# Performance work log

Hardware: AMD Instinct MI355X
Metric: run time of the kernel (lower is better)

The kernel has to match this reference:

```python
import jax, jax.numpy as jnp
import numpy as np

NUM_HEADS = 16
LN_EPS = 1e-5


def _layer_norm(x, g, b):
    m = x.mean(-1, keepdims=True)
    v = x.var(-1, keepdims=True)
    return (x - m) / jnp.sqrt(v + LN_EPS) * g + b


def setup_inputs() -> dict:
    key = jax.random.key(0)
    ks = jax.random.split(key, 4)
    Bq, Bk, Nk, C = 128, 128, 256, 1024
    return {
        "qx": jax.random.normal(ks[0], (Bq, 1, C), jnp.float32),
        "kx": jax.random.normal(ks[1], (Bk, Nk, C), jnp.float32),
        "gq": jnp.ones((C,), jnp.float32),
        "bq": jnp.zeros((C,), jnp.float32),
        "gk": jnp.ones((C,), jnp.float32),
        "bk": jnp.zeros((C,), jnp.float32),
        "Wq": jax.random.normal(ks[2], (C, C), jnp.float32) * (C ** -0.5),
        "Wk": jax.random.normal(ks[3], (C, C), jnp.float32) * (C ** -0.5),
    }


def reference(qx, kx, gq, bq, gk, bk, Wq, Wk):
    H = NUM_HEADS
    Bq, _, C = qx.shape  # qx: [Bq, 1, C]
    Bk, Nk, _ = kx.shape  # kx: [Bk, Nk, C]
    hd = C // H
    scale = hd ** -0.5
    # LayerNorm + linear projections (nn.Linear: x @ W.T, no bias)
    q = (_layer_norm(qx, gq, bq) @ Wq.T).reshape(Bq, H, hd)       # [Bq, H, hd] (Nq=1 squeezed)
    k = (_layer_norm(kx, gk, bk) @ Wk.T).reshape(Bk, Nk, H, hd)   # [Bk, Nk, H, hd]
    # Full bipartite cross-batch attention scores: [Bq, Bk, H, Nk]
    attn = jnp.einsum('qhc,knhc->qkhn', q, k) * scale
    attn = jax.nn.softmax(attn, axis=-1)
    # v = kx broadcast over heads in original einsum 'khnc,qkhn->qkc';
    # equivalent: sum attn over heads, then contract over Nk.
    w = attn.sum(axis=2)                                           # [Bq, Bk, Nk]
    x = jnp.einsum('knc,qkn->qkc', kx, w)                          # [Bq, Bk, C]
    return x
```

## Files before the change

kernel.cpp:

```cpp
#include <hip/hip_runtime.h>


typedef unsigned short ushort_t;
typedef __bf16 bf16x8 __attribute__((ext_vector_type(8)));
typedef float f32x4 __attribute__((ext_vector_type(4)));

#define AS1 __attribute__((address_space(1)))
#define AS3 __attribute__((address_space(3)))

__device__ __forceinline__ void gload_lds16(const void* g, void* l) {
  __builtin_amdgcn_global_load_lds((const AS1 unsigned int*)g, (AS3 unsigned int*)l, 16, 0, 0);
}

__device__ __forceinline__ ushort_t f2bf(float f) {
  unsigned u = __float_as_uint(f);
  unsigned r = u + 0x7FFFu + ((u >> 16) & 1u);
  return (ushort_t)(r >> 16);
}

__global__ __launch_bounds__(256) void cvt_bf16_kernel(const float* __restrict__ src,
                                                       ushort_t* __restrict__ dst, int n4) {
  int i = blockIdx.x * 256 + threadIdx.x;
  if (i < n4) {
    float4 v = ((const float4*)src)[i];
    ushort4 o;
    o.x = f2bf(v.x); o.y = f2bf(v.y); o.z = f2bf(v.z); o.w = f2bf(v.w);
    ((ushort4*)dst)[i] = o;
  }
}

__global__ __launch_bounds__(256) void ln_kernel(const float* __restrict__ kx,
                                                 const float* __restrict__ qx,
                                                 const float* __restrict__ gk,
                                                 const float* __restrict__ bk,
                                                 const float* __restrict__ gq,
                                                 const float* __restrict__ bq,
                                                 const float* __restrict__ WqF,
                                                 ushort_t* __restrict__ kln,
                                                 ushort_t* __restrict__ qproj) {
  const int tid = threadIdx.x, lane = tid & 63, wid = tid >> 6;

  if (blockIdx.x < 128) {
    const int ti = blockIdx.x * 4 + wid;
    const int mq = ti >> 6, nq = ti & 63;
    const int g = lane >> 4, rr = lane & 15;

    float s = 0.f, s2 = 0.f;
    {
      const float* p = qx + (size_t)(mq * 16 + (lane & 15)) * 1024 + (lane >> 4) * 256;
      #pragma unroll 8
      for (int i = 0; i < 64; ++i) {
        float4 v = ((const float4*)p)[i];
        s  += v.x + v.y + v.z + v.w;
        s2 += v.x*v.x + v.y*v.y + v.z*v.z + v.w*v.w;
      }
    }
    s  += __shfl_xor(s, 16);  s2 += __shfl_xor(s2, 16);
    s  += __shfl_xor(s, 32);  s2 += __shfl_xor(s2, 32);
    const float mean = s * (1.0f / 1024.0f);
    const float var  = s2 * (1.0f / 1024.0f) - mean * mean;
    const float rstd = rsqrtf(var + 1e-5f);

    const float* qa = qx  + (size_t)(mq * 16 + rr) * 1024;
    const float* wb = WqF + (size_t)(nq * 16 + rr) * 1024;

    f32x4 qacc0 = (f32x4){0.f, 0.f, 0.f, 0.f};
    f32x4 qacc1 = (f32x4){0.f, 0.f, 0.f, 0.f};
    #pragma unroll 4
    for (int kk = 0; kk < 32; kk += 2) {
      #pragma unroll
      for (int e = 0; e < 2; ++e) {
        const int co = (kk + e) * 32 + g * 8;
        float4 a0 = *(const float4*)(qa + co);
        float4 a1 = *(const float4*)(qa + co + 4);
        float4 g0 = *(const float4*)(gq + co);
        float4 g1 = *(const float4*)(gq + co + 4);
        float4 b0 = *(const float4*)(bq + co);
        float4 b1 = *(const float4*)(bq + co + 4);
        float4 w0 = *(const float4*)(wb + co);
        float4 w1 = *(const float4*)(wb + co + 4);
        bf16x8 af, bf;
        af[0] = (__bf16)((a0.x - mean) * rstd * g0.x + b0.x);
        af[1] = (__bf16)((a0.y - mean) * rstd * g0.y + b0.y);
        af[2] = (__bf16)((a0.z - mean) * rstd * g0.z + b0.z);
        af[3] = (__bf16)((a0.w - mean) * rstd * g0.w + b0.w);
        af[4] = (__bf16)((a1.x - mean) * rstd * g1.x + b1.x);
        af[5] = (__bf16)((a1.y - mean) * rstd * g1.y + b1.y);
        af[6] = (__bf16)((a1.z - mean) * rstd * g1.z + b1.z);
        af[7] = (__bf16)((a1.w - mean) * rstd * g1.w + b1.w);
        bf[0] = (__bf16)w0.x; bf[1] = (__bf16)w0.y; bf[2] = (__bf16)w0.z; bf[3] = (__bf16)w0.w;
        bf[4] = (__bf16)w1.x; bf[5] = (__bf16)w1.y; bf[6] = (__bf16)w1.z; bf[7] = (__bf16)w1.w;
        if (e == 0) qacc0 = __builtin_amdgcn_mfma_f32_16x16x32_bf16(af, bf, qacc0, 0, 0, 0);
        else        qacc1 = __builtin_amdgcn_mfma_f32_16x16x32_bf16(af, bf, qacc1, 0, 0, 0);
      }
    }
    #pragma unroll
    for (int rg = 0; rg < 4; ++rg)
      qproj[(size_t)(mq * 16 + (g << 2) + rg) * 1024 + nq * 16 + rr] =
          f2bf(qacc0[rg] + qacc1[rg]);
    return;
  }

  const int row = (blockIdx.x - 128) * 4 + wid;
  const float* src = kx + (size_t)row * 1024;
  ushort_t* dst = kln + (size_t)row * 1024;
  const int c0 = lane * 4;

  float4 v0 = *(const float4*)(src + c0);
  float4 v1 = *(const float4*)(src + c0 + 256);
  float4 v2 = *(const float4*)(src + c0 + 512);
  float4 v3 = *(const float4*)(src + c0 + 768);

  float s  = (v0.x + v0.y + v0.z + v0.w) + (v1.x + v1.y + v1.z + v1.w)
           + (v2.x + v2.y + v2.z + v2.w) + (v3.x + v3.y + v3.z + v3.w);
  float s2 = (v0.x*v0.x + v0.y*v0.y + v0.z*v0.z + v0.w*v0.w)
           + (v1.x*v1.x + v1.y*v1.y + v1.z*v1.z + v1.w*v1.w)
           + (v2.x*v2.x + v2.y*v2.y + v2.z*v2.z + v2.w*v2.w)
           + (v3.x*v3.x + v3.y*v3.y + v3.z*v3.z + v3.w*v3.w);
  #pragma unroll
  for (int off = 1; off < 64; off <<= 1) {
    s  += __shfl_xor(s, off);
    s2 += __shfl_xor(s2, off);
  }
  const float mean = s * (1.0f / 1024.0f);
  const float var  = s2 * (1.0f / 1024.0f) - mean * mean;
  const float rstd = rsqrtf(var + 1e-5f);

  float4 g0 = *(const float4*)(gk + c0);
  float4 g1 = *(const float4*)(gk + c0 + 256);
  float4 g2 = *(const float4*)(gk + c0 + 512);
  float4 g3 = *(const float4*)(gk + c0 + 768);
  float4 b0 = *(const float4*)(bk + c0);
  float4 b1 = *(const float4*)(bk + c0 + 256);
  float4 b2 = *(const float4*)(bk + c0 + 512);
  float4 b3 = *(const float4*)(bk + c0 + 768);

  ushort4 o0, o1, o2, o3;
  o0.x = f2bf((v0.x - mean) * rstd * g0.x + b0.x);
  o0.y = f2bf((v0.y - mean) * rstd * g0.y + b0.y);
  o0.z = f2bf((v0.z - mean) * rstd * g0.z + b0.z);
  o0.w = f2bf((v0.w - mean) * rstd * g0.w + b0.w);
  o1.x = f2bf((v1.x - mean) * rstd * g1.x + b1.x);
  o1.y = f2bf((v1.y - mean) * rstd * g1.y + b1.y);
  o1.z = f2bf((v1.z - mean) * rstd * g1.z + b1.z);
  o1.w = f2bf((v1.w - mean) * rstd * g1.w + b1.w);
  o2.x = f2bf((v2.x - mean) * rstd * g2.x + b2.x);
  o2.y = f2bf((v2.y - mean) * rstd * g2.y + b2.y);
  o2.z = f2bf((v2.z - mean) * rstd * g2.z + b2.z);
  o2.w = f2bf((v2.w - mean) * rstd * g2.w + b2.w);
  o3.x = f2bf((v3.x - mean) * rstd * g3.x + b3.x);
  o3.y = f2bf((v3.y - mean) * rstd * g3.y + b3.y);
  o3.z = f2bf((v3.z - mean) * rstd * g3.z + b3.z);
  o3.w = f2bf((v3.w - mean) * rstd * g3.w + b3.w);

  *(ushort4*)(dst + c0)       = o0;
  *(ushort4*)(dst + c0 + 256) = o1;
  *(ushort4*)(dst + c0 + 512) = o2;
  *(ushort4*)(dst + c0 + 768) = o3;
}

__global__ __launch_bounds__(512, 2) void gemm256_kernel(const ushort_t* __restrict__ A,
                                                         const ushort_t* __restrict__ Bt,
                                                         ushort_t* __restrict__ Cpk,
                                                         int M, int N) {
  __shared__ ushort_t Abuf[3][16384];
  __shared__ ushort_t Bbuf[2][16384];

  const int tid = threadIdx.x, lane = tid & 63, wid = tid >> 6;
  const int g = lane >> 4, rr = lane & 15;
  const int wr = wid >> 2, wc = wid & 3;

  const int Mt = M >> 8, Nt = N >> 8;
  const int nwg = Mt * Nt;
  const int qq = nwg >> 3, r8 = nwg & 7;
  const int xcd = blockIdx.x & 7, idx = blockIdx.x >> 3;
  const int wg = (xcd < r8 ? xcd * (qq + 1) : r8 * (qq + 1) + (xcd - r8) * qq) + idx;
  const int mt = wg / Nt, nt = wg - mt * Nt;
  const size_t m0 = (size_t)mt << 8, n0 = (size_t)nt << 8;

  const ushort_t* Abase = A  + m0 * 1024;
  const ushort_t* Bbase = Bt + n0 * 1024;

  f32x4 acc[8][4];
  #pragma unroll
  for (int i = 0; i < 8; ++i)
    #pragma unroll
    for (int j = 0; j < 4; ++j) acc[i][j] = (f32x4){0.f, 0.f, 0.f, 0.f};

  auto stA = [&](int kt) {
    ushort_t* dst = &Abuf[kt % 3][0];
    #pragma unroll
    for (int l = 0; l < 4; ++l) {
      int ix = l * 512 + tid;
      int r  = ix >> 3;
      int gs = (ix & 7) ^ (((r >> 2) & 1) << 1);
      gload_lds16(Abase + (size_t)r * 1024 + (kt << 6) + (gs << 3), dst + ix * 8);
    }
  };
  auto stB = [&](int kt) {
    ushort_t* dst = &Bbuf[kt & 1][0];
    #pragma unroll
    for (int l = 0; l < 4; ++l) {
      int ix = l * 512 + tid;
      int r  = ix >> 3;
      int gs = (ix & 7) ^ (((r >> 2) & 1) << 1);
      gload_lds16(Bbase + (size_t)r * 1024 + (kt << 6) + (gs << 3), dst + ix * 8);
    }
  };

  stA(0); stB(0); stA(1);
  asm volatile("s_waitcnt vmcnt(4)" ::: "memory");
  __builtin_amdgcn_s_barrier();

  const int sw = ((rr >> 2) & 1) << 1;

  #pragma unroll 1
  for (int j = 0; j < 16; ++j) {
    const ushort_t* as = &Abuf[j % 3][0];
    const ushort_t* bs = &Bbuf[j & 1][0];

    {
      bf16x8 af[8], bf[4];
      #pragma unroll
      for (int i = 0; i < 8; ++i) {
        int r = (wr << 7) + (i << 4) + rr;
        af[i] = *(const bf16x8*)&as[(r << 6) + ((g ^ sw) << 3)];
      }
      #pragma unroll
      for (int jj = 0; jj < 4; ++jj) {
        int r = (wc << 6) + (jj << 4) + rr;
        bf[jj] = *(const bf16x8*)&bs[(r << 6) + ((g ^ sw) << 3)];
      }
      if (j < 15) stB(j + 1);
      if (j < 14) stA(j + 2);
      __builtin_amdgcn_s_setprio(1);
      #pragma unroll
      for (int i = 0; i < 8; ++i)
        #pragma unroll
        for (int jj = 0; jj < 4; ++jj)
          acc[i][jj] = __builtin_amdgcn_mfma_f32_16x16x32_bf16(af[i], bf[jj], acc[i][jj], 0, 0, 0);
      __builtin_amdgcn_s_setprio(0);
    }
    {
      bf16x8 af[8], bf[4];
      #pragma unroll
      for (int i = 0; i < 8; ++i) {
        int r = (wr << 7) + (i << 4) + rr;
        af[i] = *(const bf16x8*)&as[(r << 6) + (((4 + g) ^ sw) << 3)];
      }
      #pragma unroll
      for (int jj = 0; jj < 4; ++jj) {
        int r = (wc << 6) + (jj << 4) + rr;
        bf[jj] = *(const bf16x8*)&bs[(r << 6) + (((4 + g) ^ sw) << 3)];
      }
      __builtin_amdgcn_s_setprio(1);
      #pragma unroll
      for (int i = 0; i < 8; ++i)
        #pragma unroll
        for (int jj = 0; jj < 4; ++jj)
          acc[i][jj] = __builtin_amdgcn_mfma_f32_16x16x32_bf16(af[i], bf[jj], acc[i][jj], 0, 0, 0);
      __builtin_amdgcn_s_setprio(0);
      if (j < 14) {
        asm volatile("s_waitcnt vmcnt(4)" ::: "memory");
        __builtin_amdgcn_s_barrier();
      } else if (j == 14) {
        asm volatile("s_waitcnt vmcnt(0)" ::: "memory");
        __builtin_amdgcn_s_barrier();
      }
    }
  }

  #pragma unroll
  for (int i = 0; i < 8; ++i)
    #pragma unroll
    for (int j = 0; j < 4; ++j)
      #pragma unroll
      for (int rg = 0; rg < 4; ++rg) {
        size_t row = m0 + (wr << 7) + (i << 4) + (g << 2) + rg;
        size_t col = n0 + (wc << 6) + (j << 4) + rr;
        int kb = (int)(row >> 8), t = (int)((row >> 4) & 15), r16 = (int)(row & 15);
        int h = (int)(col >> 6), ch = (int)(col & 63);
        size_t odx = ((((size_t)kb * 16 + h) * 16 + t) << 10)
                   + ((ch >> 5) << 9) + (((ch >> 3) & 3) << 7) + (r16 << 3) + (ch & 7);
        Cpk[odx] = f2bf(acc[i][j][rg]);
      }
}

__global__ __launch_bounds__(256, 3) void scores_kernel(const ushort_t* __restrict__ qp,
                                                        const ushort_t* __restrict__ kpk,
                                                        ushort_t* __restrict__ wbuf) {
  __shared__ float pbuf[2][16][258];

  const int tid = threadIdx.x, lane = tid & 63, wid = tid >> 6;
  const int g = lane >> 4, rr = lane & 15;

  const int b = blockIdx.x;
  const int wg = (b & 7) * 128 + (b >> 3);
  const int kb = wg >> 3;
  const int q0 = (wg & 7) << 4;

  const int hs = wid;

  float w_acc[16][4];
  #pragma unroll
  for (int t = 0; t < 16; ++t)
    #pragma unroll
    for (int r = 0; r < 4; ++r) w_acc[t][r] = 0.f;

  const ushort_t* qrow = qp + (size_t)(q0 + rr) * 1024;
  const ushort_t* kbb  = kpk + ((size_t)kb * 16) * 16384 + g * 128 + rr * 8;

  for (int hp = 0; hp < 4; ++hp) {
    const int h = hp * 4 + hs;
    const int co = h * 64 + g * 8;
    bf16x8 aq0 = *(const bf16x8*)(qrow + co);
    bf16x8 aq1 = *(const bf16x8*)(qrow + co + 32);
    const ushort_t* hb = kbb + (size_t)h * 16384;
    f32x4 s[16];
    #pragma unroll
    for (int t = 0; t < 16; ++t) {
      bf16x8 b0 = *(const bf16x8*)(hb + t * 1024);
      bf16x8 b1 = *(const bf16x8*)(hb + t * 1024 + 512);
      f32x4 a = (f32x4){0.f, 0.f, 0.f, 0.f};
      a = __builtin_amdgcn_mfma_f32_16x16x32_bf16(aq0, b0, a, 0, 0, 0);
      a = __builtin_amdgcn_mfma_f32_16x16x32_bf16(aq1, b1, a, 0, 0, 0);
      s[t] = a;
    }
    #pragma unroll
    for (int r = 0; r < 4; ++r) {
      float mx = s[0][r];
      #pragma unroll
      for (int t = 1; t < 16; ++t) mx = fmaxf(mx, s[t][r]);
      mx = fmaxf(mx, __shfl_xor(mx, 1));
      mx = fmaxf(mx, __shfl_xor(mx, 2));
      mx = fmaxf(mx, __shfl_xor(mx, 4));
      mx = fmaxf(mx, __shfl_xor(mx, 8));
      float sum = 0.f;
      float e[16];
      #pragma unroll
      for (int t = 0; t < 16; ++t) {
        e[t] = __expf((s[t][r] - mx) * 0.125f);
        sum += e[t];
      }
      sum += __shfl_xor(sum, 1);
      sum += __shfl_xor(sum, 2);
      sum += __shfl_xor(sum, 4);
      sum += __shfl_xor(sum, 8);
      float inv = 1.0f / sum;
      #pragma unroll
      for (int t = 0; t < 16; ++t) w_acc[t][r] += e[t] * inv;
    }
  }

  __syncthreads();
  if (hs >= 2) {
    #pragma unroll
    for (int t = 0; t < 16; ++t)
      #pragma unroll
      for (int r = 0; r < 4; ++r)
        pbuf[hs - 2][(g << 2) + r][t * 16 + rr] = w_acc[t][r];
  }
  __syncthreads();
  if (hs < 2) {
    #pragma unroll
    for (int t = 0; t < 16; ++t)
      #pragma unroll
      for (int r = 0; r < 4; ++r)
        w_acc[t][r] += pbuf[hs][(g << 2) + r][t * 16 + rr];
    if (hs == 1) {
      #pragma unroll
      for (int t = 0; t < 16; ++t)
        #pragma unroll
        for (int r = 0; r < 4; ++r)
          pbuf[1][(g << 2) + r][t * 16 + rr] = w_acc[t][r];
    }
  }
  __syncthreads();
  if (hs == 0) {
    ushort_t* wb = wbuf + (size_t)kb * 32768;
    #pragma unroll
    for (int t = 0; t < 16; ++t)
      #pragma unroll
      for (int r = 0; r < 4; ++r) {
        float v = w_acc[t][r] + pbuf[1][(g << 2) + r][t * 16 + rr];
        wb[(size_t)(q0 + (g << 2) + r) * 256 + t * 16 + rr] = f2bf(v);
      }
  }
}

__global__ __launch_bounds__(256, 4) void pv_kernel(const ushort_t* __restrict__ wbuf,
                                                    const float* __restrict__ kx,
                                                    float* __restrict__ xout) {
  const int tid = threadIdx.x, lane = tid & 63, wid = tid >> 6;
  const int g = lane >> 4, rr = lane & 15;

  const int b = blockIdx.x;
  const int wg = (b & 7) * 128 + (b >> 3);
  const int kb = wg >> 3;
  const int c0 = (wg & 7) * 128;

  const int wr = wid >> 1, wc = wid & 1;

  f32x4 acc[4][4];
  #pragma unroll
  for (int i = 0; i < 4; ++i)
    #pragma unroll
    for (int j = 0; j < 4; ++j) acc[i][j] = (f32x4){0.f, 0.f, 0.f, 0.f};

  const ushort_t* wb = wbuf + (size_t)kb * 32768;
  const float* kxb = kx + (size_t)kb * 256 * 1024;

  for (int nc = 0; nc < 8; ++nc) {
    const int n0 = nc * 32 + g * 8;
    bf16x8 af[4];
    #pragma unroll
    for (int i = 0; i < 4; ++i) {
      int q = (wr << 6) + (i << 4) + rr;
      af[i] = *(const bf16x8*)(wb + (size_t)q * 256 + n0);
    }
    #pragma unroll
    for (int j = 0; j < 4; ++j) {
      int c = c0 + (wc << 6) + (j << 4) + rr;
      const float* src = kxb + (size_t)n0 * 1024 + c;
      float f[8];
      #pragma unroll
      for (int jj = 0; jj < 8; ++jj) f[jj] = src[(size_t)jj * 1024];
      bf16x8 bb;
      #pragma unroll
      for (int jj = 0; jj < 8; ++jj) bb[jj] = (__bf16)f[jj];
      #pragma unroll
      for (int i = 0; i < 4; ++i)
        acc[i][j] = __builtin_amdgcn_mfma_f32_16x16x32_bf16(af[i], bb, acc[i][j], 0, 0, 0);
    }
  }

  #pragma unroll
  for (int i = 0; i < 4; ++i)
    #pragma unroll
    for (int j = 0; j < 4; ++j)
      #pragma unroll
      for (int rg = 0; rg < 4; ++rg) {
        int q = (wr << 6) + (i << 4) + (g << 2) + rg;
        int c = c0 + (wc << 6) + (j << 4) + rr;
        xout[((size_t)q * 128 + kb) * 1024 + c] = acc[i][j][rg];
      }
}

extern "C" void kernel_launch(void* const* d_in, const int* in_sizes, int n_in,
                              void* d_out, int out_size, void* d_ws, size_t ws_size,
                              hipStream_t stream) {
  const float* qx = (const float*)d_in[0];
  const float* kx = (const float*)d_in[1];
  const float* gq = (const float*)d_in[2];
  const float* bq = (const float*)d_in[3];
  const float* gk = (const float*)d_in[4];
  const float* bk = (const float*)d_in[5];
  const float* Wq = (const float*)d_in[6];
  const float* Wk = (const float*)d_in[7];

  char* ws = (char*)d_ws;
  ushort_t* kkp   = (ushort_t*)(ws);
  ushort_t* qproj = (ushort_t*)(ws + 67108864);
  ushort_t* wbuf  = (ushort_t*)(ws + 67371008);
  ushort_t* Wkb   = (ushort_t*)(ws + 67371008 + 2359296);
  ushort_t* kln  = (ushort_t*)d_out;
  float*    xout = (float*)d_out;

  cvt_bf16_kernel<<<1024, 256, 0, stream>>>(Wk, Wkb, 262144);
  ln_kernel<<<128 + 8192, 256, 0, stream>>>(kx, qx, gk, bk, gq, bq, Wq, kln, qproj);
  gemm256_kernel<<<512, 512, 0, stream>>>(kln, Wkb, kkp, 32768, 1024);
  scores_kernel<<<1024, 256, 0, stream>>>(qproj, kkp, wbuf);
  pv_kernel<<<1024, 256, 0, stream>>>(wbuf, kx, xout);
}
```

Baseline: 265.7 us.

## Move Q projection GEMM from LN kernel into tail of main K GEMM

The Q projection no longer runs inside the layernorm kernel as 128 blocks doing fp32 loads with inline conversion. Instead, Q is layer-normed to bf16 alongside K, Wq is converted to bf16 by a separate launch, and 64 of the 512 gemm256 workgroups compute the Q-projection tiles after their main epilogue. The aim is to take the slow fp32-load Q work off the LN kernel's critical path and spread it across the GEMM grid. The cost is an extra conversion launch, tail imbalance in the GEMM for the workgroups that take on Q work, and qln reusing wbuf workspace, which is safe only because scores writes wbuf later.

```diff
diff --git a/kernel.cpp b/kernel.cpp
--- a/kernel.cpp
+++ b/kernel.cpp
@@ -35,75 +35,18 @@
                                                  const float* __restrict__ bk,
                                                  const float* __restrict__ gq,
                                                  const float* __restrict__ bq,
-                                                 const float* __restrict__ WqF,
                                                  ushort_t* __restrict__ kln,
-                                                 ushort_t* __restrict__ qproj) {
+                                                 ushort_t* __restrict__ qln) {
   const int tid = threadIdx.x, lane = tid & 63, wid = tid >> 6;
 
-  if (blockIdx.x < 128) {
-    const int ti = blockIdx.x * 4 + wid;
-    const int mq = ti >> 6, nq = ti & 63;
-    const int g = lane >> 4, rr = lane & 15;
-
-    float s = 0.f, s2 = 0.f;
-    {
-      const float* p = qx + (size_t)(mq * 16 + (lane & 15)) * 1024 + (lane >> 4) * 256;
-      #pragma unroll 8
-      for (int i = 0; i < 64; ++i) {
-        float4 v = ((const float4*)p)[i];
-        s  += v.x + v.y + v.z + v.w;
-        s2 += v.x*v.x + v.y*v.y + v.z*v.z + v.w*v.w;
-      }
-    }
-    s  += __shfl_xor(s, 16);  s2 += __shfl_xor(s2, 16);
-    s  += __shfl_xor(s, 32);  s2 += __shfl_xor(s2, 32);
-    const float mean = s * (1.0f / 1024.0f);
-    const float var  = s2 * (1.0f / 1024.0f) - mean * mean;
-    const float rstd = rsqrtf(var + 1e-5f);
-
-    const float* qa = qx  + (size_t)(mq * 16 + rr) * 1024;
-    const float* wb = WqF + (size_t)(nq * 16 + rr) * 1024;
-
-    f32x4 qacc0 = (f32x4){0.f, 0.f, 0.f, 0.f};
-    f32x4 qacc1 = (f32x4){0.f, 0.f, 0.f, 0.f};
-    #pragma unroll 4
-    for (int kk = 0; kk < 32; kk += 2) {
-      #pragma unroll
-      for (int e = 0; e < 2; ++e) {
-        const int co = (kk + e) * 32 + g * 8;
-        float4 a0 = *(const float4*)(qa + co);
-        float4 a1 = *(const float4*)(qa + co + 4);
-        float4 g0 = *(const float4*)(gq + co);
-        float4 g1 = *(const float4*)(gq + co + 4);
-        float4 b0 = *(const float4*)(bq + co);
-        float4 b1 = *(const float4*)(bq + co + 4);
-        float4 w0 = *(const float4*)(wb + co);
-        float4 w1 = *(const float4*)(wb + co + 4);
-        bf16x8 af, bf;
-        af[0] = (__bf16)((a0.x - mean) * rstd * g0.x + b0.x);
-        af[1] = (__bf16)((a0.y - mean) * rstd * g0.y + b0.y);
-        af[2] = (__bf16)((a0.z - mean) * rstd * g0.z + b0.z);
-        af[3] = (__bf16)((a0.w - mean) * rstd * g0.w + b0.w);
-        af[4] = (__bf16)((a1.x - mean) * rstd * g1.x + b1.x);
-        af[5] = (__bf16)((a1.y - mean) * rstd * g1.y + b1.y);
-        af[6] = (__bf16)((a1.z - mean) * rstd * g1.z + b1.z);
-        af[7] = (__bf16)((a1.w - mean) * rstd * g1.w + b1.w);
-        bf[0] = (__bf16)w0.x; bf[1] = (__bf16)w0.y; bf[2] = (__bf16)w0.z; bf[3] = (__bf16)w0.w;
-        bf[4] = (__bf16)w1.x; bf[5] = (__bf16)w1.y; bf[6] = (__bf16)w1.z; bf[7] = (__bf16)w1.w;
-        if (e == 0) qacc0 = __builtin_amdgcn_mfma_f32_16x16x32_bf16(af, bf, qacc0, 0, 0, 0);
-        else        qacc1 = __builtin_amdgcn_mfma_f32_16x16x32_bf16(af, bf, qacc1, 0, 0, 0);
-      }
-    }
-    #pragma unroll
-    for (int rg = 0; rg < 4; ++rg)
-      qproj[(size_t)(mq * 16 + (g << 2) + rg) * 1024 + nq * 16 + rr] =
-          f2bf(qacc0[rg] + qacc1[rg]);
-    return;
-  }
-
-  const int row = (blockIdx.x - 128) * 4 + wid;
-  const float* src = kx + (size_t)row * 1024;
-  ushort_t* dst = kln + (size_t)row * 1024;
+  const float* src; ushort_t* dst; const float* gp; const float* bp;
+  if (blockIdx.x < 8192) {
+    const int row = blockIdx.x * 4 + wid;
+    src = kx + (size_t)row * 1024; dst = kln + (size_t)row * 1024; gp = gk; bp = bk;
+  } else {
+    const int row = (blockIdx.x - 8192) * 4 + wid;
+    src = qx + (size_t)row * 1024; dst = qln + (size_t)row * 1024; gp = gq; bp = bq;
+  }
   const int c0 = lane * 4;
 
   float4 v0 = *(const float4*)(src + c0);
@@ -126,14 +69,14 @@
   const float var  = s2 * (1.0f / 1024.0f) - mean * mean;
   const float rstd = rsqrtf(var + 1e-5f);
 
-  float4 g0 = *(const float4*)(gk + c0);
-  float4 g1 = *(const float4*)(gk + c0 + 256);
-  float4 g2 = *(const float4*)(gk + c0 + 512);
-  float4 g3 = *(const float4*)(gk + c0 + 768);
-  float4 b0 = *(const float4*)(bk + c0);
-  float4 b1 = *(const float4*)(bk + c0 + 256);
-  float4 b2 = *(const float4*)(bk + c0 + 512);
-  float4 b3 = *(const float4*)(bk + c0 + 768);
+  float4 g0 = *(const float4*)(gp + c0);
+  float4 g1 = *(const float4*)(gp + c0 + 256);
+  float4 g2 = *(const float4*)(gp + c0 + 512);
+  float4 g3 = *(const float4*)(gp + c0 + 768);
+  float4 b0 = *(const float4*)(bp + c0);
+  float4 b1 = *(const float4*)(bp + c0 + 256);
+  float4 b2 = *(const float4*)(bp + c0 + 512);
+  float4 b3 = *(const float4*)(bp + c0 + 768);
 
   ushort4 o0, o1, o2, o3;
   o0.x = f2bf((v0.x - mean) * rstd * g0.x + b0.x);
@@ -162,6 +105,9 @@
 __global__ __launch_bounds__(512, 2) void gemm256_kernel(const ushort_t* __restrict__ A,
                                                          const ushort_t* __restrict__ Bt,
                                                          ushort_t* __restrict__ Cpk,
+                                                         const ushort_t* __restrict__ qA,
+                                                         const ushort_t* __restrict__ qB,
+                                                         ushort_t* __restrict__ qC,
                                                          int M, int N) {
   __shared__ ushort_t Abuf[3][16384];
   __shared__ ushort_t Bbuf[2][16384];
@@ -284,6 +230,27 @@
                    + ((ch >> 5) << 9) + (((ch >> 3) & 3) << 7) + (r16 << 3) + (ch & 7);
         Cpk[odx] = f2bf(acc[i][j][rg]);
       }
+
+  if ((wg & 63) < 8) {
+    const int ti = ((wg >> 6) << 6) + ((wg & 7) << 3) + wid;
+    const int mq = ti >> 6, nq = ti & 63;
+    const ushort_t* qa = qA + (size_t)(mq * 16 + rr) * 1024 + g * 8;
+    const ushort_t* qb = qB + (size_t)(nq * 16 + rr) * 1024 + g * 8;
+    f32x4 qacc0 = (f32x4){0.f, 0.f, 0.f, 0.f};
+    f32x4 qacc1 = (f32x4){0.f, 0.f, 0.f, 0.f};
+    #pragma unroll
+    for (int kk = 0; kk < 32; kk += 2) {
+      bf16x8 a0 = *(const bf16x8*)(qa + kk * 32);
+      bf16x8 b0 = *(const bf16x8*)(qb + kk * 32);
+      bf16x8 a1 = *(const bf16x8*)(qa + kk * 32 + 32);
+      bf16x8 b1 = *(const bf16x8*)(qb + kk * 32 + 32);
+      qacc0 = __builtin_amdgcn_mfma_f32_16x16x32_bf16(a0, b0, qacc0, 0, 0, 0);
+      qacc1 = __builtin_amdgcn_mfma_f32_16x16x32_bf16(a1, b1, qacc1, 0, 0, 0);
+    }
+    #pragma unroll
+    for (int rg = 0; rg < 4; ++rg)
+      qC[(size_t)(mq * 16 + (g << 2) + rg) * 1024 + nq * 16 + rr] = f2bf(qacc0[rg] + qacc1[rg]);
+  }
 }
 
 __global__ __launch_bounds__(256, 3) void scores_kernel(const ushort_t* __restrict__ qp,
@@ -462,13 +429,16 @@
   ushort_t* kkp   = (ushort_t*)(ws);
   ushort_t* qproj = (ushort_t*)(ws + 67108864);
   ushort_t* wbuf  = (ushort_t*)(ws + 67371008);
+  ushort_t* qln   = (ushort_t*)(ws + 67371008);
+  ushort_t* Wqb   = (ushort_t*)(ws + 67371008 + 262144);
   ushort_t* Wkb   = (ushort_t*)(ws + 67371008 + 2359296);
   ushort_t* kln  = (ushort_t*)d_out;
   float*    xout = (float*)d_out;
 
+  cvt_bf16_kernel<<<1024, 256, 0, stream>>>(Wq, Wqb, 262144);
   cvt_bf16_kernel<<<1024, 256, 0, stream>>>(Wk, Wkb, 262144);
-  ln_kernel<<<128 + 8192, 256, 0, stream>>>(kx, qx, gk, bk, gq, bq, Wq, kln, qproj);
-  gemm256_kernel<<<512, 512, 0, stream>>>(kln, Wkb, kkp, 32768, 1024);
+  ln_kernel<<<8192 + 32, 256, 0, stream>>>(kx, qx, gk, bk, gq, bq, kln, qln);
+  gemm256_kernel<<<512, 512, 0, stream>>>(kln, Wkb, kkp, qln, Wqb, qproj, 32768, 1024);
   scores_kernel<<<1024, 256, 0, stream>>>(qproj, kkp, wbuf);
   pv_kernel<<<1024, 256, 0, stream>>>(wbuf, kx, xout);
 }
```

Measured after the change: 258.8 us. 1.03x faster.
